# Kernel tuning notes

Hardware: AMD Instinct MI355X
Metric: run time of the kernel (lower is better)

Reference implementation:

```python
import jax, jax.numpy as jnp
import numpy as np

MAX_DIM = 1024
VOCAB = 257
DEPTH = 6
Q_DIM = MAX_DIM // 4  # 256
EXP_DIMS = [1, 2, 4, 8, 16, 32, 64, 128]  # expander sizes: current_q doubles up to Q_DIM
BATCH, SEQ = 8, 4096


def qlinear(q, W):
    """Quaternion Hamilton-product linear.
    q: [..., in, 4] (last dim = r,i,j,k components), W: [4, out, in] (stacked r,i,j,k weights).
    Returns [..., out, 4].
    """
    # P[..., o, w, a] = F.linear(component_a, W_w)  -> all 16 small GEMMs in one einsum
    P = jnp.einsum('...ia,woi->...owa', q, W)
    Pr, Pi, Pj, Pk = P[..., 0, :], P[..., 1, :], P[..., 2, :], P[..., 3, :]  # each [..., out, 4]
    out_r = Pr[..., 0] - Pi[..., 1] - Pj[..., 2] - Pk[..., 3]
    out_i = Pi[..., 0] + Pr[..., 1] + Pk[..., 2] - Pj[..., 3]
    out_j = Pj[..., 0] - Pk[..., 1] + Pr[..., 2] + Pi[..., 3]
    out_k = Pk[..., 0] + Pj[..., 1] - Pi[..., 2] + Pr[..., 3]
    return jnp.stack([out_r, out_i, out_j, out_k], axis=-1)


def qnormalize(q):
    norm = jnp.linalg.norm(q, axis=-1, keepdims=True)
    return q / (norm + 1e-8)


def setup_inputs() -> dict:
    key = jax.random.key(0)
    ks = jax.random.split(key, 4 + len(EXP_DIMS))
    inp = {}
    inp['x'] = jax.random.randint(ks[0], (BATCH, SEQ), 0, VOCAB)
    inp['emb'] = jax.random.normal(ks[1], (VOCAB, 4), dtype=jnp.float32)
    for idx, cq in enumerate(EXP_DIMS):
        scale = cq ** (-0.5)
        inp[f'w_exp{idx}'] = jax.random.uniform(ks[2 + idx], (4, cq, cq), jnp.float32, -scale, scale)
    scale = Q_DIM ** (-0.5)
    inp['w_layers'] = jax.random.uniform(ks[-2], (DEPTH, 4, Q_DIM, Q_DIM), jnp.float32, -scale, scale)
    inp['w_head'] = jax.random.normal(ks[-1], (VOCAB, MAX_DIM), dtype=jnp.float32) * MAX_DIM ** (-0.5)
    return inp


def reference(x, emb, w_exp0, w_exp1, w_exp2, w_exp3, w_exp4, w_exp5, w_exp6, w_exp7,
              w_layers, w_head):
    q = emb[x][:, :, None, :]  # [B, S, 1, 4]
    for w in (w_exp0, w_exp1, w_exp2, w_exp3, w_exp4, w_exp5, w_exp6, w_exp7):
        delta = jnp.tanh(qlinear(q, w))
        q = jnp.concatenate([q + delta, q - delta], axis=2)  # doubles quaternion dim
    for d in range(DEPTH):
        q = qnormalize(qlinear(q, w_layers[d]))
    stability_loss = jnp.mean(jnp.abs(q[..., 0]))
    h_flat = q.reshape(x.shape[0], x.shape[1], -1)  # [B, S, MAX_DIM]
    logits = jnp.einsum('bsd,vd->bsv', h_flat, w_head)
    return (logits, stability_loss)
```

## Files before the change

### kernel.cpp

```cpp
#include <hip/hip_runtime.h>


typedef _Float16 f16x8 __attribute__((ext_vector_type(8)));
typedef float    f32x4 __attribute__((ext_vector_type(4)));

#define GL2LDS16(gp, lp) __builtin_amdgcn_global_load_lds(                     \
    (const __attribute__((address_space(1))) void*)(gp),                       \
    (__attribute__((address_space(3))) void*)(lp), 16, 0, 0)

#define STG(slot, isB, half, PB, kb)                                           \
  do {                                                                         \
    GL2LDS16((PB) + (size_t)(2 * (half)) * oG + (kb),                          \
             S + (slot) * 32768 + (isB) * 16384 + (half) * 8192 + tid * 8);    \
    GL2LDS16((PB) + (size_t)(2 * (half) + 1) * oG + (kb),                      \
             S + (slot) * 32768 + (isB) * 16384 + (half) * 8192 + 4096 +       \
                 tid * 8);                                                     \
  } while (0)

__device__ __forceinline__ unsigned short f2h(float f) {
  union { _Float16 h; unsigned short u; } c;
  c.h = (_Float16)f;
  return c.u;
}
__device__ __forceinline__ float h2f(unsigned short u) {
  union { unsigned short u; _Float16 h; } c;
  c.u = u;
  return (float)c.h;
}

__global__ __launch_bounds__(256) void expand_ham(
    const float* __restrict__ w, unsigned short* __restrict__ out,
    int cq, int kbits, int total) {
  int id = blockIdx.x * 256 + threadIdx.x;
  if (id >= total) return;
  const int K = 1 << kbits;
  const int n = id >> kbits;
  const int k = id & (K - 1);
  float val = 0.f;
  if (n < 4 * cq) {
    const int o = n >> 2, a = n & 3, i = k >> 2, b = k & 3;
    const int   comp[4][4] = {{0,1,2,3},{1,0,3,2},{2,3,0,1},{3,2,1,0}};
    const float sgn [4][4] = {{1.f,-1.f,-1.f,-1.f},{1.f,1.f,1.f,-1.f},
                              {1.f,-1.f,1.f,1.f},{1.f,1.f,-1.f,1.f}};
    val = sgn[a][b] * w[comp[a][b] * cq * cq + o * cq + i];
  }
  out[id] = f2h(val);
}

__global__ __launch_bounds__(256) void expand_ham6(
    const float* __restrict__ w, unsigned short* __restrict__ out) {
  const int id = blockIdx.x * 256 + threadIdx.x;
  const int d = id >> 20;
  const int r = id & 1048575;
  const int n = r >> 10, k = r & 1023;
  const int o = n >> 2, a = n & 3, i = k >> 2, b = k & 3;
  const int   comp[4][4] = {{0,1,2,3},{1,0,3,2},{2,3,0,1},{3,2,1,0}};
  const float sgn [4][4] = {{1.f,-1.f,-1.f,-1.f},{1.f,1.f,1.f,-1.f},
                            {1.f,-1.f,1.f,1.f},{1.f,1.f,-1.f,1.f}};
  const float val =
      sgn[a][b] * w[d * 262144 + comp[a][b] * 65536 + o * 256 + i];
  out[id] = f2h(val);
}

__global__ __launch_bounds__(256) void conv_head(
    const float* __restrict__ wh, unsigned short* __restrict__ out) {
  int id = blockIdx.x * 256 + threadIdx.x;
  int v = id >> 10, k = id & 1023;
  out[id] = f2h(v < 257 ? wh[v * 1024 + k] : 0.f);
}

template <int CQ>
__device__ __forceinline__ void exp_step(float (&q)[16][4],
                                         const float* __restrict__ w) {
  float d[CQ][4];
#pragma unroll
  for (int o = 0; o < CQ; o++) {
    float pr = 0.f, pi = 0.f, pj = 0.f, pk = 0.f;
#pragma unroll
    for (int i = 0; i < CQ; i++) {
      const float wr = w[0 * CQ * CQ + o * CQ + i];
      const float wi = w[1 * CQ * CQ + o * CQ + i];
      const float wj = w[2 * CQ * CQ + o * CQ + i];
      const float wk = w[3 * CQ * CQ + o * CQ + i];
      const float qr = q[i][0], qi = q[i][1], qj = q[i][2], qk = q[i][3];
      pr += wr * qr - wi * qi - wj * qj - wk * qk;
      pi += wi * qr + wr * qi + wk * qj - wj * qk;
      pj += wj * qr - wk * qi + wr * qj + wi * qk;
      pk += wk * qr + wj * qi - wi * qj + wr * qk;
    }
    d[o][0] = tanhf(pr); d[o][1] = tanhf(pi);
    d[o][2] = tanhf(pj); d[o][3] = tanhf(pk);
  }
#pragma unroll
  for (int o = 0; o < CQ; o++)
#pragma unroll
    for (int a = 0; a < 4; a++) {
      const float dd = d[o][a], qq = q[o][a];
      q[o][a]      = qq + dd;
      q[CQ + o][a] = qq - dd;
    }
}

__global__ __launch_bounds__(256) void embed_expand(
    const int* __restrict__ x, const float* __restrict__ emb,
    const float* __restrict__ w0, const float* __restrict__ w1,
    const float* __restrict__ w2, const float* __restrict__ w3,
    unsigned short* __restrict__ out) {
  const int t = blockIdx.x * 256 + threadIdx.x;
  float q[16][4];
  const int v = x[t];
  const float4 e = *(const float4*)(emb + v * 4);
  q[0][0] = e.x; q[0][1] = e.y; q[0][2] = e.z; q[0][3] = e.w;
  exp_step<1>(q, w0);
  exp_step<2>(q, w1);
  exp_step<4>(q, w2);
  exp_step<8>(q, w3);
  ushort4* o4 = (ushort4*)(out + (size_t)t * 64);
#pragma unroll
  for (int c = 0; c < 16; c++) {
    ushort4 u;
    u.x = f2h(q[c][0]); u.y = f2h(q[c][1]);
    u.z = f2h(q[c][2]); u.w = f2h(q[c][3]);
    o4[c] = u;
  }
}

__global__ __launch_bounds__(256) void gemm_epi0(
    const unsigned short* __restrict__ W,
    const unsigned short* __restrict__ Act,
    unsigned short* __restrict__ OutB,
    int K, int Nreal, int ldout) {
  __shared__ unsigned short WtL[128 * 32];
  __shared__ unsigned short WtH[128 * 32];
  __shared__ unsigned short AtL[128 * 32];
  __shared__ unsigned short AtH[128 * 32];

  const int tid  = threadIdx.x;
  const int wave = tid >> 6;
  const int lane = tid & 63;
  const int l15  = lane & 15;
  const int quad = lane >> 4;

  const int Gx = gridDim.x;
  const int L  = blockIdx.y * Gx + blockIdx.x;
  const int j  = L & 7;
  const int s  = L >> 3;
  const int nblock = (s % Gx) * 128;
  const int mblock = (32 * j + s / Gx) * 128;
  const int wn = (wave & 1) * 64;
  const int wm = (wave >> 1) * 64;

  f32x4 acc[4][4];
  const f32x4 zero = {0.f, 0.f, 0.f, 0.f};
#pragma unroll
  for (int a = 0; a < 4; a++)
#pragma unroll
    for (int b = 0; b < 4; b++) acc[a][b] = zero;

  const int row0 = tid >> 2;
  const int sub  = tid & 3;
  const unsigned short* gW0 = W   + (size_t)(nblock + row0)      * K + sub * 8;
  const unsigned short* gW1 = W   + (size_t)(nblock + row0 + 64) * K + sub * 8;
  const unsigned short* gA0 = Act + (size_t)(mblock + row0)      * K + sub * 8;
  const unsigned short* gA1 = Act + (size_t)(mblock + row0 + 64) * K + sub * 8;
  unsigned short* lWL0 = &WtL[wave * 512];
  unsigned short* lWL1 = &WtL[2048 + wave * 512];
  unsigned short* lWH0 = &WtH[wave * 512];
  unsigned short* lWH1 = &WtH[2048 + wave * 512];
  unsigned short* lAL0 = &AtL[wave * 512];
  unsigned short* lAL1 = &AtL[2048 + wave * 512];
  unsigned short* lAH0 = &AtH[wave * 512];
  unsigned short* lAH1 = &AtH[2048 + wave * 512];

  for (int kb = 0; kb < K; kb += 64) {
    GL2LDS16(gW0 + kb,      lWL0);
    GL2LDS16(gW1 + kb,      lWL1);
    GL2LDS16(gW0 + kb + 32, lWH0);
    GL2LDS16(gW1 + kb + 32, lWH1);
    GL2LDS16(gA0 + kb,      lAL0);
    GL2LDS16(gA1 + kb,      lAL1);
    GL2LDS16(gA0 + kb + 32, lAH0);
    GL2LDS16(gA1 + kb + 32, lAH1);
    __syncthreads();

    {
      f16x8 afr[4], bfr[4];
#pragma unroll
      for (int tn = 0; tn < 4; tn++)
        afr[tn] = *(const f16x8*)&WtL[(wn + tn * 16 + l15) * 32 + quad * 8];
#pragma unroll
      for (int tm = 0; tm < 4; tm++)
        bfr[tm] = *(const f16x8*)&AtL[(wm + tm * 16 + l15) * 32 + quad * 8];
#pragma unroll
      for (int tn = 0; tn < 4; tn++)
#pragma unroll
        for (int tm = 0; tm < 4; tm++)
          acc[tn][tm] = __builtin_amdgcn_mfma_f32_16x16x32_f16(
              afr[tn], bfr[tm], acc[tn][tm], 0, 0, 0);
    }
    {
      f16x8 afr[4], bfr[4];
#pragma unroll
      for (int tn = 0; tn < 4; tn++)
        afr[tn] = *(const f16x8*)&WtH[(wn + tn * 16 + l15) * 32 + quad * 8];
#pragma unroll
      for (int tm = 0; tm < 4; tm++)
        bfr[tm] = *(const f16x8*)&AtH[(wm + tm * 16 + l15) * 32 + quad * 8];
#pragma unroll
      for (int tn = 0; tn < 4; tn++)
#pragma unroll
        for (int tm = 0; tm < 4; tm++)
          acc[tn][tm] = __builtin_amdgcn_mfma_f32_16x16x32_f16(
              afr[tn], bfr[tm], acc[tn][tm], 0, 0, 0);
    }
    __syncthreads();
  }

#pragma unroll
  for (int tn = 0; tn < 4; tn++) {
    const int n = nblock + wn + tn * 16 + quad * 4;
    if (n < Nreal) {
#pragma unroll
      for (int tm = 0; tm < 4; tm++) {
        const int token = mblock + wm + tm * 16 + l15;
        const f32x4 v = acc[tn][tm];
        const unsigned short* ip = Act + (size_t)token * K + n;
        const float i0 = h2f(ip[0]), i1 = h2f(ip[1]);
        const float i2 = h2f(ip[2]), i3 = h2f(ip[3]);
        const float d0 = tanhf(v[0]), d1 = tanhf(v[1]);
        const float d2 = tanhf(v[2]), d3 = tanhf(v[3]);
        ushort4 up, um;
        up.x = f2h(i0 + d0); up.y = f2h(i1 + d1);
        up.z = f2h(i2 + d2); up.w = f2h(i3 + d3);
        um.x = f2h(i0 - d0); um.y = f2h(i1 - d1);
        um.z = f2h(i2 - d2); um.w = f2h(i3 - d3);
        *(ushort4*)&OutB[(size_t)token * ldout + n] = up;
        *(ushort4*)&OutB[(size_t)token * ldout + Nreal + n] = um;
      }
    }
  }
}

template <int EPI>
__global__ __launch_bounds__(512, 4) void gemm8p(
    const unsigned short* __restrict__ W,
    const unsigned short* __restrict__ Act,
    unsigned short* __restrict__ OutB, float* __restrict__ OutF,
    int K, int NW, int ldout) {
  __shared__ unsigned short S[3 * 12288];
  __shared__ float lsum[8];

  const int tid  = threadIdx.x;
  const int wave = tid >> 6;
  const int lane = tid & 63;
  const int l15  = lane & 15;
  const int quad = lane >> 4;
  const int wr   = wave >> 2;
  const int wc   = wave & 3;

  const int Gx = gridDim.x;
  const int L  = blockIdx.y * Gx + blockIdx.x;
  const int j  = L & 7;
  const int s  = L >> 3;
  const int mblock = (j * (gridDim.y >> 3) + s / Gx) * 256;
  const int nblock = (s % Gx) * 128;
  const int NT = K >> 5;

  f32x4 acc[4][4];
  const f32x4 zero = {0.f, 0.f, 0.f, 0.f};
#pragma unroll
  for (int a = 0; a < 4; a++)
#pragma unroll
    for (int b = 0; b < 4; b++) acc[a][b] = zero;

  const int rw = tid >> 2;
  const int sl = (tid & 3) ^ ((tid >> 3) & 3);
  const int wrow = nblock + rw;
  const int cwr  = wrow < NW ? wrow : NW - 1;
  const unsigned short* sW  = W   + (size_t)cwr * K + sl * 8;
  const unsigned short* sB0 = Act + (size_t)(mblock + rw)       * K + sl * 8;
  const unsigned short* sB1 = Act + (size_t)(mblock + 128 + rw) * K + sl * 8;

  const int swz = (quad * 8) ^ ((l15 & 6) << 2);

#pragma unroll
  for (int t = 0; t < 2; ++t) {
    unsigned short* d = S + t * 12288 + tid * 8;
    GL2LDS16(sW  + t * 32, d);
    GL2LDS16(sB0 + t * 32, d + 4096);
    GL2LDS16(sB1 + t * 32, d + 8192);
  }
  asm volatile("s_waitcnt vmcnt(3)" ::: "memory");
  __builtin_amdgcn_s_barrier();
  __builtin_amdgcn_sched_barrier(0);

  int bC = 0;
  int bS = 2;
  for (int kt = 0; kt < NT; ++kt) {
    const unsigned short* SA = S + bC * 12288;
    const unsigned short* SB = SA + 4096;

    f16x8 af[4], bf[4];
#pragma unroll
    for (int t4 = 0; t4 < 4; t4++)
      af[t4] = *(const f16x8*)(SA + (wr * 64 + t4 * 16 + l15) * 32 + swz);
#pragma unroll
    for (int t4 = 0; t4 < 4; t4++)
      bf[t4] = *(const f16x8*)(SB + (wc * 64 + t4 * 16 + l15) * 32 + swz);

    if (kt + 2 < NT) {
      const int kb = (kt + 2) * 32;
      unsigned short* d = S + bS * 12288 + tid * 8;
      GL2LDS16(sW  + kb, d);
      GL2LDS16(sB0 + kb, d + 4096);
      GL2LDS16(sB1 + kb, d + 8192);
    }

    __builtin_amdgcn_s_barrier();
    asm volatile("s_waitcnt lgkmcnt(0)" ::: "memory");
    __builtin_amdgcn_sched_barrier(0);
    __builtin_amdgcn_s_setprio(1);
#pragma unroll
    for (int tn = 0; tn < 4; tn++)
#pragma unroll
      for (int tm = 0; tm < 4; tm++)
        acc[tn][tm] = __builtin_amdgcn_mfma_f32_16x16x32_f16(
            af[tn], bf[tm], acc[tn][tm], 0, 0, 0);
    __builtin_amdgcn_s_setprio(0);

    if (kt < NT - 1) {
      if (kt + 2 < NT) asm volatile("s_waitcnt vmcnt(3)" ::: "memory");
      else             asm volatile("s_waitcnt vmcnt(0)" ::: "memory");
      __builtin_amdgcn_s_barrier();
      __builtin_amdgcn_sched_barrier(0);
    }
    bC = bC == 2 ? 0 : bC + 1;
    bS = bS == 2 ? 0 : bS + 1;
  }

  {
    float loss = 0.f;
#pragma unroll
    for (int tn = 0; tn < 4; tn++) {
      const int n = nblock + wr * 64 + tn * 16 + quad * 4;
#pragma unroll
      for (int tm = 0; tm < 4; tm++) {
        const int token = mblock + wc * 64 + tm * 16 + l15;
        const f32x4 v = acc[tn][tm];
        const float nrm =
            sqrtf(v[0] * v[0] + v[1] * v[1] + v[2] * v[2] + v[3] * v[3]);
        const float inv = 1.f / (nrm + 1e-8f);
        ushort4 u;
        u.x = f2h(v[0] * inv); u.y = f2h(v[1] * inv);
        u.z = f2h(v[2] * inv); u.w = f2h(v[3] * inv);
        *(ushort4*)&OutB[(size_t)token * 1024 + n] = u;
        if constexpr (EPI == 2) loss += fabsf(v[0] * inv);
      }
    }
    if constexpr (EPI == 2) {
#pragma unroll
      for (int off = 32; off > 0; off >>= 1) loss += __shfl_down(loss, off);
      if (lane == 0) lsum[wave] = loss;
      __syncthreads();
      if (tid == 0) {
        float t = 0.f;
#pragma unroll
        for (int w8 = 0; w8 < 8; w8++) t += lsum[w8];
        atomicAdd(OutF, t * (1.f / 8388608.f));
      }
    }
  }
}

template <int EPI>
__global__ __launch_bounds__(512, 2) void gemm_8ph(
    const unsigned short* __restrict__ W,
    const unsigned short* __restrict__ Act,
    unsigned short* __restrict__ OutB, float* __restrict__ OutF,
    int K, int NW, int ldout) {
  __shared__ unsigned short S[65536];

  const int tid  = threadIdx.x;
  const int wave = tid >> 6;
  const int lane = tid & 63;
  const int l15  = lane & 15;
  const int quad = lane >> 4;
  const int wr   = wave >> 2;
  const int wc   = wave & 3;

  const int Gx = gridDim.x;
  const int L  = blockIdx.y * Gx + blockIdx.x;
  const int j  = L & 7;
  const int s  = L >> 3;
  const int mblock = (j * (gridDim.y >> 3) + s / Gx) * 256;
  const int nblock = (s % Gx) * 256;
  const int NI = K >> 7;

  f32x4 acc[8][4];
  const f32x4 zero = {0.f, 0.f, 0.f, 0.f};
#pragma unroll
  for (int a = 0; a < 8; a++)
#pragma unroll
    for (int b = 0; b < 4; b++) acc[a][b] = zero;

  const int r8 = tid >> 3;
  const int s8 = (tid & 7) ^ (r8 & 7);
  const size_t oG = (size_t)64 * K;
  const unsigned short* pWb = W   + (size_t)nblock * K + r8 * K + s8 * 8;
  const unsigned short* pBb = Act + (size_t)mblock * K + r8 * K + s8 * 8;

  const int lrow = l15 * 64;
  const int ksw0 = ((quad)     ^ (l15 & 7)) * 8;
  const int ksw1 = ((4 + quad) ^ (l15 & 7)) * 8;

  STG(0, 0, 0, pWb, 0);  STG(0, 0, 1, pWb, 0);
  STG(0, 1, 0, pBb, 0);  STG(0, 1, 1, pBb, 0);
  STG(1, 1, 0, pBb, 64); STG(1, 1, 1, pBb, 64);
  asm volatile("s_waitcnt vmcnt(4)" ::: "memory");
  __builtin_amdgcn_s_barrier();
  __builtin_amdgcn_sched_barrier(0);

  f16x8 bfr[4][2];
  for (int i = 0; i < NI; ++i) {
    const bool nl = (i < NI - 1);
    const int kA1 = (2 * i + 1) * 64;
    const int k2  = (2 * i + 2) * 64;
    const int k3  = (2 * i + 3) * 64;
#pragma unroll
    for (int p = 0; p < 8; ++p) {
      const int q  = p & 3;
      const int sb = (p >> 2) * 32768;
      if (q == 0) {
#pragma unroll
        for (int c = 0; c < 4; ++c) {
          const unsigned short* bp = S + sb + 16384 + (wc * 64 + c * 16) * 64
                                       + lrow;
          bfr[c][0] = *(const f16x8*)(bp + ksw0);
          bfr[c][1] = *(const f16x8*)(bp + ksw1);
        }
      }
      f16x8 af[2][2];
#pragma unroll
      for (int f = 0; f < 2; ++f) {
        const unsigned short* ap = S + sb + (wr * 128 + q * 32 + f * 16) * 64
                                     + lrow;
        af[f][0] = *(const f16x8*)(ap + ksw0);
        af[f][1] = *(const f16x8*)(ap + ksw1);
      }
      if      (p == 0) { STG(1, 0, 0, pWb, kA1); }
      else if (p == 1) { STG(1, 0, 1, pWb, kA1); }
      else if (p == 2) { if (nl) STG(0, 1, 0, pBb, k2); }
      else if (p == 3) { if (nl) STG(0, 1, 1, pBb, k2); }
      else if (p == 4) { if (nl) STG(0, 0, 0, pWb, k2); }
      else if (p == 5) { if (nl) STG(0, 0, 1, pWb, k2); }
      else if (p == 6) { if (nl) STG(1, 1, 0, pBb, k3); }
      else             { if (nl) STG(1, 1, 1, pBb, k3); }

      __builtin_amdgcn_s_barrier();
      asm volatile("s_waitcnt lgkmcnt(0)" ::: "memory");
      __builtin_amdgcn_sched_barrier(0);
      __builtin_amdgcn_s_setprio(1);
#pragma unroll
      for (int f = 0; f < 2; ++f)
#pragma unroll
        for (int c = 0; c < 4; ++c) {
          acc[q * 2 + f][c] = __builtin_amdgcn_mfma_f32_16x16x32_f16(
              af[f][0], bfr[c][0], acc[q * 2 + f][c], 0, 0, 0);
          acc[q * 2 + f][c] = __builtin_amdgcn_mfma_f32_16x16x32_f16(
              af[f][1], bfr[c][1], acc[q * 2 + f][c], 0, 0, 0);
        }
      __builtin_amdgcn_s_setprio(0);

      if (p == 3) {
        if (nl) asm volatile("s_waitcnt vmcnt(4)" ::: "memory");
        else    asm volatile("s_waitcnt vmcnt(0)" ::: "memory");
        __builtin_amdgcn_s_barrier();
        __builtin_amdgcn_sched_barrier(0);
      } else if (p == 7) {
        if (nl) {
          asm volatile("s_waitcnt vmcnt(4)" ::: "memory");
          __builtin_amdgcn_s_barrier();
          __builtin_amdgcn_sched_barrier(0);
        }
      } else {
        __builtin_amdgcn_s_barrier();
      }
    }
  }

  if constexpr (EPI == 0) {
#pragma unroll
    for (int tn = 0; tn < 8; tn++) {
      const int n = nblock + wr * 128 + tn * 16 + quad * 4;
#pragma unroll
      for (int tm = 0; tm < 4; tm++) {
        const int token = mblock + wc * 64 + tm * 16 + l15;
        const f32x4 v = acc[tn][tm];
        const unsigned short* ip = Act + (size_t)token * K + n;
        const float i0 = h2f(ip[0]), i1 = h2f(ip[1]);
        const float i2 = h2f(ip[2]), i3 = h2f(ip[3]);
        const float d0 = tanhf(v[0]), d1 = tanhf(v[1]);
        const float d2 = tanhf(v[2]), d3 = tanhf(v[3]);
        ushort4 up, um;
        up.x = f2h(i0 + d0); up.y = f2h(i1 + d1);
        up.z = f2h(i2 + d2); up.w = f2h(i3 + d3);
        um.x = f2h(i0 - d0); um.y = f2h(i1 - d1);
        um.z = f2h(i2 - d2); um.w = f2h(i3 - d3);
        *(ushort4*)&OutB[(size_t)token * ldout + n] = up;
        *(ushort4*)&OutB[(size_t)token * ldout + NW + n] = um;
      }
    }
  } else {
#pragma unroll
    for (int tn = 0; tn < 8; tn++) {
      const int n = nblock + wr * 128 + tn * 16 + quad * 4;
      if (n < 257) {
#pragma unroll
        for (int tm = 0; tm < 4; tm++) {
          const int token = mblock + wc * 64 + tm * 16 + l15;
          const f32x4 v = acc[tn][tm];
#pragma unroll
          for (int r = 0; r < 4; r++)
            if (n + r < 257) OutF[(size_t)token * 257 + n + r] = v[r];
        }
      }
    }
  }
}

extern "C" void kernel_launch(void* const* d_in, const int* in_sizes, int n_in,
                              void* d_out, int out_size, void* d_ws,
                              size_t ws_size, hipStream_t stream) {
  const int*   x    = (const int*)d_in[0];
  const float* emb  = (const float*)d_in[1];
  const float* we0  = (const float*)d_in[2];
  const float* we1  = (const float*)d_in[3];
  const float* we2  = (const float*)d_in[4];
  const float* we3  = (const float*)d_in[5];
  const float* we4  = (const float*)d_in[6];
  const float* we5  = (const float*)d_in[7];
  const float* we6  = (const float*)d_in[8];
  const float* we7  = (const float*)d_in[9];
  const float* wlay = (const float*)d_in[10];
  const float* wh   = (const float*)d_in[11];
  float* out = (float*)d_out;

  char* p = (char*)d_ws;
  auto alloc = [&](size_t bytes) {
    void* r = (void*)p;
    p += (bytes + 255) & ~(size_t)255;
    return r;
  };
  unsigned short* act0 = (unsigned short*)alloc(32768ull * 1024 * 2);
  unsigned short* act1 = (unsigned short*)alloc(32768ull * 1024 * 2);
  unsigned short* E4 = (unsigned short*)alloc(128 * 64 * 2);
  unsigned short* E5 = (unsigned short*)alloc(128 * 128 * 2);
  unsigned short* E6 = (unsigned short*)alloc(256 * 256 * 2);
  unsigned short* E7 = (unsigned short*)alloc(512 * 512 * 2);
  unsigned short* EL = (unsigned short*)alloc(6ull * 1024 * 1024 * 2);
  unsigned short* WH = (unsigned short*)alloc(512 * 1024 * 2);

  hipMemsetAsync(out + 8421376, 0, 4, stream);

  expand_ham<<<dim3(8192 / 256), 256, 0, stream>>>(we4, E4, 16, 6, 128 * 64);
  expand_ham<<<dim3(16384 / 256), 256, 0, stream>>>(we5, E5, 32, 7, 128 * 128);
  expand_ham<<<dim3(65536 / 256), 256, 0, stream>>>(we6, E6, 64, 8, 256 * 256);
  expand_ham<<<dim3(262144 / 256), 256, 0, stream>>>(we7, E7, 128, 9,
                                                     512 * 512);
  expand_ham6<<<dim3(6 * 1048576 / 256), 256, 0, stream>>>(wlay, EL);
  conv_head<<<dim3(512 * 1024 / 256), 256, 0, stream>>>(wh, WH);

  embed_expand<<<dim3(128), 256, 0, stream>>>(x, emb, we0, we1, we2, we3, act0);

  gemm_epi0<<<dim3(1, 256), 256, 0, stream>>>(E4, act0, act1, 64, 64, 128);
  gemm_epi0<<<dim3(1, 256), 256, 0, stream>>>(E5, act1, act0, 128, 128, 256);
  gemm_8ph<0><<<dim3(1, 128), 512, 0, stream>>>(E6, act0, act1, nullptr, 256,
                                                256, 512);
  gemm_8ph<0><<<dim3(2, 128), 512, 0, stream>>>(E7, act1, act0, nullptr, 512,
                                                512, 1024);

  unsigned short* a = act0;
  unsigned short* b = act1;
  for (int d = 0; d < 5; d++) {
    gemm8p<1><<<dim3(8, 128), 512, 0, stream>>>(EL + (size_t)d * 1048576, a, b,
                                                nullptr, 1024, 1024, 1024);
    unsigned short* t = a; a = b; b = t;
  }
  gemm8p<2><<<dim3(8, 128), 512, 0, stream>>>(EL + 5ull * 1048576, a, b,
                                              out + 8421376, 1024, 1024, 1024);
  { unsigned short* t = a; a = b; b = t; }

  gemm_8ph<3><<<dim3(2, 128), 512, 0, stream>>>(WH, a, nullptr, out, 1024, 0,
                                                0);
}
```

Baseline: 796.8 us.

## Add dedicated head GEMM kernel with 128-wide N tiles to cut padding

Replaces the head projection, which used the 256-wide-N gemm_8ph kernel padded to 512 vocab rows, with a new gemm_head kernel. The new kernel uses 128x256 tiles and a 3-stage LDS ring pipeline, so only 384 padded vocab rows are converted and computed. This cuts wasted MFMA work on padding and allows higher occupancy (launch bounds 4). The cost is smaller tiles and a different pipeline that may reuse operands less per load.

```diff
diff --git a/kernel.cpp b/kernel.cpp
--- a/kernel.cpp
+++ b/kernel.cpp
@@ -372,6 +372,114 @@
   }
 }
 
+__global__ __launch_bounds__(512, 4) void gemm_head(
+    const unsigned short* __restrict__ W,
+    const unsigned short* __restrict__ Act,
+    float* __restrict__ OutF, int K) {
+  __shared__ unsigned short S[3 * 12288];
+
+  const int tid  = threadIdx.x;
+  const int wave = tid >> 6;
+  const int lane = tid & 63;
+  const int l15  = lane & 15;
+  const int quad = lane >> 4;
+  const int wr   = wave >> 2;
+  const int wc   = wave & 3;
+
+  const int Gx = gridDim.x;
+  const int L  = blockIdx.y * Gx + blockIdx.x;
+  const int j  = L & 7;
+  const int s  = L >> 3;
+  const int mblock = (j * (gridDim.y >> 3) + s / Gx) * 256;
+  const int nblock = (s % Gx) * 128;
+  const int NT = K >> 5;
+
+  f32x4 acc[4][4];
+  const f32x4 zero = {0.f, 0.f, 0.f, 0.f};
+#pragma unroll
+  for (int a = 0; a < 4; a++)
+#pragma unroll
+    for (int b = 0; b < 4; b++) acc[a][b] = zero;
+
+  const int rw = tid >> 2;
+  const int sl = (tid & 3) ^ ((tid >> 3) & 3);
+  const unsigned short* sW  = W   + (size_t)(nblock + rw) * K + sl * 8;
+  const unsigned short* sB0 = Act + (size_t)(mblock + rw)       * K + sl * 8;
+  const unsigned short* sB1 = Act + (size_t)(mblock + 128 + rw) * K + sl * 8;
+
+  const int swz = (quad * 8) ^ ((l15 & 6) << 2);
+
+#pragma unroll
+  for (int t = 0; t < 2; ++t) {
+    unsigned short* d = S + t * 12288 + tid * 8;
+    GL2LDS16(sW  + t * 32, d);
+    GL2LDS16(sB0 + t * 32, d + 4096);
+    GL2LDS16(sB1 + t * 32, d + 8192);
+  }
+  asm volatile("s_waitcnt vmcnt(3)" ::: "memory");
+  __builtin_amdgcn_s_barrier();
+  __builtin_amdgcn_sched_barrier(0);
+
+  int bC = 0;
+  int bS = 2;
+  for (int kt = 0; kt < NT; ++kt) {
+    const unsigned short* SA = S + bC * 12288;
+    const unsigned short* SB = SA + 4096;
+
+    f16x8 af[4], bf[4];
+#pragma unroll
+    for (int t4 = 0; t4 < 4; t4++)
+      af[t4] = *(const f16x8*)(SA + (wr * 64 + t4 * 16 + l15) * 32 + swz);
+#pragma unroll
+    for (int t4 = 0; t4 < 4; t4++)
+      bf[t4] = *(const f16x8*)(SB + (wc * 64 + t4 * 16 + l15) * 32 + swz);
+
+    if (kt + 2 < NT) {
+      const int kb = (kt + 2) * 32;
+      unsigned short* d = S + bS * 12288 + tid * 8;
+      GL2LDS16(sW  + kb, d);
+      GL2LDS16(sB0 + kb, d + 4096);
+      GL2LDS16(sB1 + kb, d + 8192);
+    }
+
+    __builtin_amdgcn_s_barrier();
+    asm volatile("s_waitcnt lgkmcnt(0)" ::: "memory");
+    __builtin_amdgcn_sched_barrier(0);
+    __builtin_amdgcn_s_setprio(1);
+#pragma unroll
+    for (int tn = 0; tn < 4; tn++)
+#pragma unroll
+      for (int tm = 0; tm < 4; tm++)
+        acc[tn][tm] = __builtin_amdgcn_mfma_f32_16x16x32_f16(
+            af[tn], bf[tm], acc[tn][tm], 0, 0, 0);
+    __builtin_amdgcn_s_setprio(0);
+
+    if (kt < NT - 1) {
+      if (kt + 2 < NT) asm volatile("s_waitcnt vmcnt(3)" ::: "memory");
+      else             asm volatile("s_waitcnt vmcnt(0)" ::: "memory");
+      __builtin_amdgcn_s_barrier();
+      __builtin_amdgcn_sched_barrier(0);
+    }
+    bC = bC == 2 ? 0 : bC + 1;
+    bS = bS == 2 ? 0 : bS + 1;
+  }
+
+#pragma unroll
+  for (int tn = 0; tn < 4; tn++) {
+    const int n = nblock + wr * 64 + tn * 16 + quad * 4;
+    if (n < 257) {
+#pragma unroll
+      for (int tm = 0; tm < 4; tm++) {
+        const int token = mblock + wc * 64 + tm * 16 + l15;
+        const f32x4 v = acc[tn][tm];
+#pragma unroll
+        for (int r = 0; r < 4; r++)
+          if (n + r < 257) OutF[(size_t)token * 257 + n + r] = v[r];
+      }
+    }
+  }
+}
+
 template <int EPI>
 __global__ __launch_bounds__(512, 2) void gemm_8ph(
     const unsigned short* __restrict__ W,
@@ -488,42 +596,25 @@
     }
   }
 
-  if constexpr (EPI == 0) {
-#pragma unroll
-    for (int tn = 0; tn < 8; tn++) {
-      const int n = nblock + wr * 128 + tn * 16 + quad * 4;
-#pragma unroll
-      for (int tm = 0; tm < 4; tm++) {
-        const int token = mblock + wc * 64 + tm * 16 + l15;
-        const f32x4 v = acc[tn][tm];
-        const unsigned short* ip = Act + (size_t)token * K + n;
-        const float i0 = h2f(ip[0]), i1 = h2f(ip[1]);
-        const float i2 = h2f(ip[2]), i3 = h2f(ip[3]);
-        const float d0 = tanhf(v[0]), d1 = tanhf(v[1]);
-        const float d2 = tanhf(v[2]), d3 = tanhf(v[3]);
-        ushort4 up, um;
-        up.x = f2h(i0 + d0); up.y = f2h(i1 + d1);
-        up.z = f2h(i2 + d2); up.w = f2h(i3 + d3);
-        um.x = f2h(i0 - d0); um.y = f2h(i1 - d1);
-        um.z = f2h(i2 - d2); um.w = f2h(i3 - d3);
-        *(ushort4*)&OutB[(size_t)token * ldout + n] = up;
-        *(ushort4*)&OutB[(size_t)token * ldout + NW + n] = um;
-      }
-    }
-  } else {
-#pragma unroll
-    for (int tn = 0; tn < 8; tn++) {
-      const int n = nblock + wr * 128 + tn * 16 + quad * 4;
-      if (n < 257) {
-#pragma unroll
-        for (int tm = 0; tm < 4; tm++) {
-          const int token = mblock + wc * 64 + tm * 16 + l15;
-          const f32x4 v = acc[tn][tm];
-#pragma unroll
-          for (int r = 0; r < 4; r++)
-            if (n + r < 257) OutF[(size_t)token * 257 + n + r] = v[r];
-        }
-      }
+#pragma unroll
+  for (int tn = 0; tn < 8; tn++) {
+    const int n = nblock + wr * 128 + tn * 16 + quad * 4;
+#pragma unroll
+    for (int tm = 0; tm < 4; tm++) {
+      const int token = mblock + wc * 64 + tm * 16 + l15;
+      const f32x4 v = acc[tn][tm];
+      const unsigned short* ip = Act + (size_t)token * K + n;
+      const float i0 = h2f(ip[0]), i1 = h2f(ip[1]);
+      const float i2 = h2f(ip[2]), i3 = h2f(ip[3]);
+      const float d0 = tanhf(v[0]), d1 = tanhf(v[1]);
+      const float d2 = tanhf(v[2]), d3 = tanhf(v[3]);
+      ushort4 up, um;
+      up.x = f2h(i0 + d0); up.y = f2h(i1 + d1);
+      up.z = f2h(i2 + d2); up.w = f2h(i3 + d3);
+      um.x = f2h(i0 - d0); um.y = f2h(i1 - d1);
+      um.z = f2h(i2 - d2); um.w = f2h(i3 - d3);
+      *(ushort4*)&OutB[(size_t)token * ldout + n] = up;
+      *(ushort4*)&OutB[(size_t)token * ldout + NW + n] = um;
     }
   }
 }
@@ -558,7 +649,7 @@
   unsigned short* E6 = (unsigned short*)alloc(256 * 256 * 2);
   unsigned short* E7 = (unsigned short*)alloc(512 * 512 * 2);
   unsigned short* EL = (unsigned short*)alloc(6ull * 1024 * 1024 * 2);
-  unsigned short* WH = (unsigned short*)alloc(512 * 1024 * 2);
+  unsigned short* WH = (unsigned short*)alloc(384 * 1024 * 2);
 
   hipMemsetAsync(out + 8421376, 0, 4, stream);
 
@@ -568,7 +659,7 @@
   expand_ham<<<dim3(262144 / 256), 256, 0, stream>>>(we7, E7, 128, 9,
                                                      512 * 512);
   expand_ham6<<<dim3(6 * 1048576 / 256), 256, 0, stream>>>(wlay, EL);
-  conv_head<<<dim3(512 * 1024 / 256), 256, 0, stream>>>(wh, WH);
+  conv_head<<<dim3(384 * 1024 / 256), 256, 0, stream>>>(wh, WH);
 
   embed_expand<<<dim3(128), 256, 0, stream>>>(x, emb, we0, we1, we2, we3, act0);
 
@@ -590,6 +681,5 @@
                                               out + 8421376, 1024, 1024, 1024);
   { unsigned short* t = a; a = b; b = t; }
 
-  gemm_8ph<3><<<dim3(2, 128), 512, 0, stream>>>(WH, a, nullptr, out, 1024, 0,
-                                                0);
-}
+  gemm_head<<<dim3(3, 128), 512, 0, stream>>>(WH, a, out, 1024);
+}
```

After: 834.4 us. 1.05x slower.
